# Optimization experiments

Hardware: AMD Instinct MI355X
Metric: run time of the kernel (lower is better)

The kernel has to match this reference:

```python
import jax, jax.numpy as jnp
import numpy as np

IN_C = 256
OUT_C = 256
HID = IN_C * 2
N_POINTS = 262144
N_NODES = 8192
B = 16
MAX_NODES = 512
EPS = 1e-5


def _mlp(h, w1, b1, g1, be1, w2, b2):
    # PyG MLP([C, 2C, out], norm='layer_norm'): lin -> layernorm -> relu -> (dropout, eval=identity) -> lin
    h = h @ w1 + b1
    mu = jnp.mean(h, axis=-1, keepdims=True)
    var = jnp.var(h, axis=-1, keepdims=True)
    h = (h - mu) * jax.lax.rsqrt(var + EPS) * g1 + be1
    h = jax.nn.relu(h)
    return h @ w2 + b2


def setup_inputs() -> dict:
    key = jax.random.key(0)
    ks = jax.random.split(key, 16)
    x = jax.random.normal(ks[0], (N_POINTS, IN_C), dtype=jnp.float32)
    f_point_batches = jnp.sort(jax.random.randint(ks[1], (N_POINTS,), 0, N_NODES)).astype(jnp.int32)
    # equal-sized graphs (16 graphs x 512 nodes), sorted as torch.split/pad_sequence assume
    g_node_batches = jnp.repeat(jnp.arange(B, dtype=jnp.int32), MAX_NODES)
    s = 1.0 / np.sqrt(IN_C)
    s2 = 1.0 / np.sqrt(HID)
    def lin(k, fan_in, shape, scale):
        return jax.random.uniform(k, shape, jnp.float32, -scale, scale)
    params = {}
    for i, name in enumerate(['Wq', 'Wk']):
        base = 2 + i * 6
        params[f'{name}_w1'] = lin(ks[base + 0], IN_C, (IN_C, HID), s)
        params[f'{name}_b1'] = lin(ks[base + 1], IN_C, (HID,), s)
        params[f'{name}_g1'] = jnp.ones((HID,), jnp.float32)
        params[f'{name}_be1'] = jnp.zeros((HID,), jnp.float32)
        params[f'{name}_w2'] = lin(ks[base + 2], HID, (HID, OUT_C), s2)
        params[f'{name}_b2'] = lin(ks[base + 3], HID, (OUT_C,), s2)
    return dict(x=x, f_point_batches=f_point_batches, g_node_batches=g_node_batches,
                num_graphs=B, max_nodes=MAX_NODES, **params)


def reference(x, f_point_batches, g_node_batches, num_graphs, max_nodes,
              Wq_w1, Wq_b1, Wq_g1, Wq_be1, Wq_w2, Wq_b2,
              Wk_w1, Wk_b1, Wk_g1, Wk_be1, Wk_w2, Wk_b2):
    n_nodes = g_node_batches.shape[0]
    C = x.shape[1]
    # scatter_mean over points -> per-node feature means [n_nodes, C]
    sums = jax.ops.segment_sum(x, f_point_batches, num_segments=n_nodes)
    cnt = jax.ops.segment_sum(jnp.ones((x.shape[0],), x.dtype), f_point_batches, num_segments=n_nodes)
    mean = sums / jnp.maximum(cnt, 1.0)[:, None]
    # ragged split by graph + pad_sequence -> [B, max_nodes, C]
    starts = jnp.searchsorted(g_node_batches, jnp.arange(num_graphs, dtype=g_node_batches.dtype))
    pos = jnp.arange(n_nodes) - starts[g_node_batches]
    padded = jnp.zeros((num_graphs, max_nodes, C), x.dtype).at[g_node_batches, pos].set(mean, mode='drop')
    q = _mlp(padded, Wq_w1, Wq_b1, Wq_g1, Wq_be1, Wq_w2, Wq_b2)  # [B, MAXN, out]
    k = _mlp(padded, Wk_w1, Wk_b1, Wk_g1, Wk_be1, Wk_w2, Wk_b2)
    return jnp.einsum('bnd,bmd->bnm', q, k)  # bmm(q, k^T)
```

## Files before the change

### kernel.cpp

```cpp
#include <hip/hip_runtime.h>
#include <hip/hip_bf16.h>

#define N_POINTS 262144
#define N_NODES  8192
#define IN_C     256
#define HID      512
#define OUT_C    256
#define NB       16
#define MAXN     512
#define EPSV     1e-5f
#define NPB      16

typedef __attribute__((ext_vector_type(8))) short short8;
typedef __attribute__((ext_vector_type(4))) float f32x4;
#define MFMA16(a, b, c) __builtin_amdgcn_mfma_f32_16x16x32_bf16((a), (b), (c), 0, 0, 0)


__global__ __launch_bounds__(256) void prelude_k(
    const int* __restrict__ fpb, int* __restrict__ starts,
    const float* __restrict__ W1q, const float* __restrict__ W1k,
    const float* __restrict__ W2q, const float* __restrict__ W2k,
    __hip_bfloat16* __restrict__ P1q, __hip_bfloat16* __restrict__ P1k,
    __hip_bfloat16* __restrict__ P2q, __hip_bfloat16* __restrict__ P2k)
{
  if (blockIdx.x < 1024) {
    const int i = blockIdx.x * 256 + threadIdx.x;
    const int cur = fpb[i];
    const int prev = (i == 0) ? -1 : fpb[i - 1];
    for (int n = prev + 1; n <= cur; ++n) starts[n] = i;
    if (i == N_POINTS - 1)
      for (int n = cur + 1; n <= N_NODES; ++n) starts[n] = N_POINTS;
    return;
  }
  const int bid = blockIdx.x - 1024;
  const int sel = bid >> 6;
  const float* W; __hip_bfloat16* P; int N;
  switch (sel) {
    case 0:  W = W1q; P = P1q; N = HID;   break;
    case 1:  W = W1k; P = P1k; N = HID;   break;
    case 2:  W = W2q; P = P2q; N = OUT_C; break;
    default: W = W2k; P = P2k; N = OUT_C; break;
  }
  const int idx = (bid & 63) * 256 + threadIdx.x;
  const int NF = N >> 4;
  const int lane = idx & 63;
  const int nf = (idx >> 6) % NF;
  const int ks = idx / (64 * NF);
  const int k0 = ks * 32 + (lane >> 4) * 8;
  const int n  = nf * 16 + (lane & 15);
  __hip_bfloat16 tmp[8];
  #pragma unroll
  for (int j = 0; j < 8; ++j) tmp[j] = __float2bfloat16(W[(size_t)(k0 + j) * N + n]);
  *(uint4*)(P + (size_t)idx * 8) = *(uint4*)tmp;
}

__global__ __launch_bounds__(512, 4) void fused_mlp_k(
    const float* __restrict__ x, const int* __restrict__ starts,
    const __hip_bfloat16* __restrict__ P1q, const __hip_bfloat16* __restrict__ P2q,
    const float* __restrict__ b1q, const float* __restrict__ g1q,
    const float* __restrict__ be1q, const float* __restrict__ b2q,
    const __hip_bfloat16* __restrict__ P1k, const __hip_bfloat16* __restrict__ P2k,
    const float* __restrict__ b1k, const float* __restrict__ g1k,
    const float* __restrict__ be1k, const float* __restrict__ b2k,
    __hip_bfloat16* __restrict__ qo, __hip_bfloat16* __restrict__ ko)
{
  const int n0 = blockIdx.x * NPB;
  const int t = threadIdx.x;
  const int w = t >> 6, l = t & 63, lg = l >> 4, lm = l & 15;
  const int h = w >> 2;
  const int c = w & 3;

  const __hip_bfloat16* P1 = h ? P1k : P1q;
  const __hip_bfloat16* P2 = h ? P2k : P2q;
  const float* b1  = h ? b1k  : b1q;
  const float* g1  = h ? g1k  : g1q;
  const float* be1 = h ? be1k : be1q;
  const float* b2  = h ? b2k  : b2q;
  __hip_bfloat16* out = h ? ko : qo;

  __shared__ __hip_bfloat16 As[NPB * 264];
  __shared__ __hip_bfloat16 Hs[2][NPB * 520];
  __shared__ float lnp[8][NPB][2];

  #pragma unroll
  for (int i = 0; i < 2; ++i) {
    const int nl = w * 2 + i;
    const int node = n0 + nl;
    const int s_ = starts[node], e_ = starts[node + 1];
    float4 a0 = make_float4(0.f, 0.f, 0.f, 0.f);
    float4 a1 = a0, a2 = a0, a3 = a0;
    int r = s_;
    for (; r + 4 <= e_; r += 4) {
      float4 v0 = *(const float4*)(x + (size_t)(r + 0) * IN_C + l * 4);
      float4 v1 = *(const float4*)(x + (size_t)(r + 1) * IN_C + l * 4);
      float4 v2 = *(const float4*)(x + (size_t)(r + 2) * IN_C + l * 4);
      float4 v3 = *(const float4*)(x + (size_t)(r + 3) * IN_C + l * 4);
      a0.x += v0.x; a0.y += v0.y; a0.z += v0.z; a0.w += v0.w;
      a1.x += v1.x; a1.y += v1.y; a1.z += v1.z; a1.w += v1.w;
      a2.x += v2.x; a2.y += v2.y; a2.z += v2.z; a2.w += v2.w;
      a3.x += v3.x; a3.y += v3.y; a3.z += v3.z; a3.w += v3.w;
    }
    for (; r < e_; ++r) {
      float4 v = *(const float4*)(x + (size_t)r * IN_C + l * 4);
      a0.x += v.x; a0.y += v.y; a0.z += v.z; a0.w += v.w;
    }
    a0.x += a1.x + a2.x + a3.x;
    a0.y += a1.y + a2.y + a3.y;
    a0.z += a1.z + a2.z + a3.z;
    a0.w += a1.w + a2.w + a3.w;
    const int cnt = e_ - s_;
    const float inv = cnt > 0 ? 1.0f / (float)cnt : 0.0f;
    __hip_bfloat16 o[4];
    o[0] = __float2bfloat16(a0.x * inv);
    o[1] = __float2bfloat16(a0.y * inv);
    o[2] = __float2bfloat16(a0.z * inv);
    o[3] = __float2bfloat16(a0.w * inv);
    *(uint2*)(As + nl * 264 + l * 4) = *(uint2*)o;
  }
  __syncthreads();

  f32x4 acc1[8];
  #pragma unroll
  for (int nj = 0; nj < 8; ++nj)
    #pragma unroll
    for (int r = 0; r < 4; ++r) acc1[nj][r] = 0.f;

  for (int ks = 0; ks < 8; ++ks) {
    short8 a = *(const short8*)(As + lm * 264 + ks * 32 + lg * 8);
    const __hip_bfloat16* bp = P1 + ((size_t)(ks * 32 + c * 8) * 64 + l) * 8;
    #pragma unroll
    for (int nj = 0; nj < 8; ++nj) {
      short8 b = *(const short8*)(bp + (size_t)nj * 512);
      acc1[nj] = MFMA16(a, b, acc1[nj]);
    }
  }

  float b1v[8], g1v[8], e1v[8];
  #pragma unroll
  for (int nj = 0; nj < 8; ++nj) {
    const int col = c * 128 + nj * 16 + lm;
    b1v[nj] = b1[col]; g1v[nj] = g1[col]; e1v[nj] = be1[col];
  }
  #pragma unroll
  for (int nj = 0; nj < 8; ++nj)
    #pragma unroll
    for (int r = 0; r < 4; ++r) acc1[nj][r] += b1v[nj];

  #pragma unroll
  for (int r = 0; r < 4; ++r) {
    float s = 0.f, q = 0.f;
    #pragma unroll
    for (int nj = 0; nj < 8; ++nj) {
      const float v = acc1[nj][r];
      s += v; q += v * v;
    }
    #pragma unroll
    for (int off = 1; off < 16; off <<= 1) {
      s += __shfl_xor(s, off);
      q += __shfl_xor(q, off);
    }
    if (lm == 0) {
      const int row = lg * 4 + r;
      lnp[w][row][0] = s;
      lnp[w][row][1] = q;
    }
  }
  __syncthreads();

  #pragma unroll
  for (int r = 0; r < 4; ++r) {
    const int row = lg * 4 + r;
    float S = 0.f, Q = 0.f;
    #pragma unroll
    for (int w2 = 0; w2 < 4; ++w2) {
      S += lnp[h * 4 + w2][row][0];
      Q += lnp[h * 4 + w2][row][1];
    }
    const float mu = S * (1.0f / HID);
    const float rs = rsqrtf(Q * (1.0f / HID) - mu * mu + EPSV);
    #pragma unroll
    for (int nj = 0; nj < 8; ++nj) {
      const float y = (acc1[nj][r] - mu) * rs * g1v[nj] + e1v[nj];
      Hs[h][row * 520 + c * 128 + nj * 16 + lm] = __float2bfloat16(fmaxf(y, 0.f));
    }
  }
  __syncthreads();

  f32x4 acc2[4];
  #pragma unroll
  for (int nj = 0; nj < 4; ++nj)
    #pragma unroll
    for (int r = 0; r < 4; ++r) acc2[nj][r] = 0.f;

  for (int ks = 0; ks < 16; ++ks) {
    short8 a = *(const short8*)(Hs[h] + lm * 520 + ks * 32 + lg * 8);
    const __hip_bfloat16* bp = P2 + ((size_t)(ks * 16 + c * 4) * 64 + l) * 8;
    #pragma unroll
    for (int nj = 0; nj < 4; ++nj) {
      short8 b = *(const short8*)(bp + (size_t)nj * 512);
      acc2[nj] = MFMA16(a, b, acc2[nj]);
    }
  }

  float b2v[4];
  #pragma unroll
  for (int nj = 0; nj < 4; ++nj) b2v[nj] = b2[c * 64 + nj * 16 + lm];
  #pragma unroll
  for (int nj = 0; nj < 4; ++nj)
    #pragma unroll
    for (int r = 0; r < 4; ++r) {
      const int row = n0 + lg * 4 + r;
      const int col = c * 64 + nj * 16 + lm;
      out[(size_t)row * OUT_C + col] = __float2bfloat16(acc2[nj][r] + b2v[nj]);
    }
}

__global__ __launch_bounds__(256, 4) void bmm_k(
    const __hip_bfloat16* __restrict__ q, const __hip_bfloat16* __restrict__ k,
    float* __restrict__ out)
{
  const int b  = blockIdx.z;
  const int n0 = blockIdx.x * 64;
  const int m0 = blockIdx.y * 64;
  const int t = threadIdx.x;
  const int w = t >> 6, l = t & 63, lg = l >> 4, lm = l & 15;

  const __hip_bfloat16* qb = q + ((size_t)b * MAXN + n0 + w * 16) * OUT_C;
  const __hip_bfloat16* kb = k + ((size_t)b * MAXN + m0) * OUT_C;

  f32x4 acc[4];
  #pragma unroll
  for (int nj = 0; nj < 4; ++nj)
    #pragma unroll
    for (int r = 0; r < 4; ++r) acc[nj][r] = 0.f;

  for (int ks = 0; ks < 8; ++ks) {
    short8 a = *(const short8*)(qb + (size_t)lm * OUT_C + ks * 32 + lg * 8);
    #pragma unroll
    for (int nj = 0; nj < 4; ++nj) {
      short8 bb = *(const short8*)(kb + (size_t)(nj * 16 + lm) * OUT_C + ks * 32 + lg * 8);
      acc[nj] = MFMA16(a, bb, acc[nj]);
    }
  }

  #pragma unroll
  for (int nj = 0; nj < 4; ++nj)
    #pragma unroll
    for (int r = 0; r < 4; ++r) {
      const int nrow = n0 + w * 16 + lg * 4 + r;
      const int mcol = m0 + nj * 16 + lm;
      out[((size_t)b * MAXN + nrow) * MAXN + mcol] = acc[nj][r];
    }
}

extern "C" void kernel_launch(void* const* d_in, const int* in_sizes, int n_in,
                              void* d_out, int out_size, void* d_ws, size_t ws_size,
                              hipStream_t stream)
{
  const float* x   = (const float*)d_in[0];
  const int*   fpb = (const int*)d_in[1];
  const float* Wq_w1  = (const float*)d_in[5];
  const float* Wq_b1  = (const float*)d_in[6];
  const float* Wq_g1  = (const float*)d_in[7];
  const float* Wq_be1 = (const float*)d_in[8];
  const float* Wq_w2  = (const float*)d_in[9];
  const float* Wq_b2  = (const float*)d_in[10];
  const float* Wk_w1  = (const float*)d_in[11];
  const float* Wk_b1  = (const float*)d_in[12];
  const float* Wk_g1  = (const float*)d_in[13];
  const float* Wk_be1 = (const float*)d_in[14];
  const float* Wk_w2  = (const float*)d_in[15];
  const float* Wk_b2  = (const float*)d_in[16];

  __hip_bfloat16* ws = (__hip_bfloat16*)d_ws;
  __hip_bfloat16* P1q  = ws;
  __hip_bfloat16* P1k  = P1q + 131072;
  __hip_bfloat16* P2q  = P1k + 131072;
  __hip_bfloat16* P2k  = P2q + 131072;
  __hip_bfloat16* qo   = P2k + 131072;
  __hip_bfloat16* ko   = qo + 2097152;
  int* starts = (int*)(ko + 2097152);
  float* out = (float*)d_out;

  prelude_k<<<1280, 256, 0, stream>>>(fpb, starts,
      Wq_w1, Wk_w1, Wq_w2, Wk_w2, P1q, P1k, P2q, P2k);
  fused_mlp_k<<<N_NODES / NPB, 512, 0, stream>>>(
      x, starts, P1q, P2q, Wq_b1, Wq_g1, Wq_be1, Wq_b2,
      P1k, P2k, Wk_b1, Wk_g1, Wk_be1, Wk_b2, qo, ko);
  bmm_k<<<dim3(8, 8, NB), 256, 0, stream>>>(qo, ko, out);
}
```

Before: 89.92 us.

## Warp-specialize fused MLP into producer and consumer waves with double-buffered tiles

The fused MLP kernel now runs 1024-thread blocks split into 8 producer waves that compute scatter-mean node features and 8 consumer waves that run the two MFMA GEMMs with layernorm. Each block handles two 16-node tiles, double-buffered in shared memory, so the memory-bound gather of x for the next tile overlaps with the matrix math of the previous one. The cost is halving the number of blocks, adding extra barriers per iteration, and a pipeline prologue and epilogue where half the waves sit idle. Occupancy may also drop because of the larger block and shared memory footprint.

```diff
diff --git a/kernel.cpp b/kernel.cpp
--- a/kernel.cpp
+++ b/kernel.cpp
@@ -13,6 +13,7 @@
 
 typedef __attribute__((ext_vector_type(8))) short short8;
 typedef __attribute__((ext_vector_type(4))) float f32x4;
+typedef __attribute__((ext_vector_type(4))) float f4v;
 #define MFMA16(a, b, c) __builtin_amdgcn_mfma_f32_16x16x32_bf16((a), (b), (c), 0, 0, 0)
 
 
@@ -54,7 +55,23 @@
   *(uint4*)(P + (size_t)idx * 8) = *(uint4*)tmp;
 }
 
-__global__ __launch_bounds__(512, 4) void fused_mlp_k(
+__device__ __forceinline__ void accum_rows(
+    const float* __restrict__ x, int lo, int hi, int l,
+    f4v& a0, f4v& a1, f4v& a2, f4v& a3)
+{
+  int r = lo;
+  for (; r + 4 <= hi; r += 4) {
+    f4v v0 = *(const f4v*)(x + (size_t)(r + 0) * IN_C + l * 4);
+    f4v v1 = *(const f4v*)(x + (size_t)(r + 1) * IN_C + l * 4);
+    f4v v2 = *(const f4v*)(x + (size_t)(r + 2) * IN_C + l * 4);
+    f4v v3 = *(const f4v*)(x + (size_t)(r + 3) * IN_C + l * 4);
+    a0 += v0; a1 += v1; a2 += v2; a3 += v3;
+  }
+  for (; r < hi; ++r)
+    a0 += *(const f4v*)(x + (size_t)r * IN_C + l * 4);
+}
+
+__global__ __launch_bounds__(1024) void fused_mlp_k(
     const float* __restrict__ x, const int* __restrict__ starts,
     const __hip_bfloat16* __restrict__ P1q, const __hip_bfloat16* __restrict__ P2q,
     const float* __restrict__ b1q, const float* __restrict__ g1q,
@@ -64,155 +81,169 @@
     const float* __restrict__ be1k, const float* __restrict__ b2k,
     __hip_bfloat16* __restrict__ qo, __hip_bfloat16* __restrict__ ko)
 {
-  const int n0 = blockIdx.x * NPB;
   const int t = threadIdx.x;
-  const int w = t >> 6, l = t & 63, lg = l >> 4, lm = l & 15;
-  const int h = w >> 2;
-  const int c = w & 3;
+  const int wv = t >> 6;
+  const int l = t & 63, lg = l >> 4, lm = l & 15;
+  const bool prod = wv < 8;
+  const int pw = wv & 7;
+  const int cw = wv & 7;
+  const int h = cw >> 2;
+  const int c = cw & 3;
+  const int n0b = blockIdx.x * (2 * NPB);
+
+  __shared__ __hip_bfloat16 As[2][NPB * 264];
+  __shared__ __hip_bfloat16 Hs[2][NPB * 520];
+  __shared__ float lnp[8][NPB][2];
 
   const __hip_bfloat16* P1 = h ? P1k : P1q;
   const __hip_bfloat16* P2 = h ? P2k : P2q;
-  const float* b1  = h ? b1k  : b1q;
-  const float* g1  = h ? g1k  : g1q;
-  const float* be1 = h ? be1k : be1q;
-  const float* b2  = h ? b2k  : b2q;
-  __hip_bfloat16* out = h ? ko : qo;
-
-  __shared__ __hip_bfloat16 As[NPB * 264];
-  __shared__ __hip_bfloat16 Hs[2][NPB * 520];
-  __shared__ float lnp[8][NPB][2];
-
-  #pragma unroll
-  for (int i = 0; i < 2; ++i) {
-    const int nl = w * 2 + i;
-    const int node = n0 + nl;
-    const int s_ = starts[node], e_ = starts[node + 1];
-    float4 a0 = make_float4(0.f, 0.f, 0.f, 0.f);
-    float4 a1 = a0, a2 = a0, a3 = a0;
-    int r = s_;
-    for (; r + 4 <= e_; r += 4) {
-      float4 v0 = *(const float4*)(x + (size_t)(r + 0) * IN_C + l * 4);
-      float4 v1 = *(const float4*)(x + (size_t)(r + 1) * IN_C + l * 4);
-      float4 v2 = *(const float4*)(x + (size_t)(r + 2) * IN_C + l * 4);
-      float4 v3 = *(const float4*)(x + (size_t)(r + 3) * IN_C + l * 4);
-      a0.x += v0.x; a0.y += v0.y; a0.z += v0.z; a0.w += v0.w;
-      a1.x += v1.x; a1.y += v1.y; a1.z += v1.z; a1.w += v1.w;
-      a2.x += v2.x; a2.y += v2.y; a2.z += v2.z; a2.w += v2.w;
-      a3.x += v3.x; a3.y += v3.y; a3.z += v3.z; a3.w += v3.w;
-    }
-    for (; r < e_; ++r) {
-      float4 v = *(const float4*)(x + (size_t)r * IN_C + l * 4);
-      a0.x += v.x; a0.y += v.y; a0.z += v.z; a0.w += v.w;
-    }
-    a0.x += a1.x + a2.x + a3.x;
-    a0.y += a1.y + a2.y + a3.y;
-    a0.z += a1.z + a2.z + a3.z;
-    a0.w += a1.w + a2.w + a3.w;
-    const int cnt = e_ - s_;
-    const float inv = cnt > 0 ? 1.0f / (float)cnt : 0.0f;
-    __hip_bfloat16 o[4];
-    o[0] = __float2bfloat16(a0.x * inv);
-    o[1] = __float2bfloat16(a0.y * inv);
-    o[2] = __float2bfloat16(a0.z * inv);
-    o[3] = __float2bfloat16(a0.w * inv);
-    *(uint2*)(As + nl * 264 + l * 4) = *(uint2*)o;
-  }
-  __syncthreads();
-
-  f32x4 acc1[8];
-  #pragma unroll
-  for (int nj = 0; nj < 8; ++nj)
-    #pragma unroll
-    for (int r = 0; r < 4; ++r) acc1[nj][r] = 0.f;
-
-  for (int ks = 0; ks < 8; ++ks) {
-    short8 a = *(const short8*)(As + lm * 264 + ks * 32 + lg * 8);
-    const __hip_bfloat16* bp = P1 + ((size_t)(ks * 32 + c * 8) * 64 + l) * 8;
+  __hip_bfloat16* outp = h ? ko : qo;
+
+  float b1v[8], g1v[8], e1v[8], b2v[4];
+  if (!prod) {
+    const float* b1  = h ? b1k  : b1q;
+    const float* g1  = h ? g1k  : g1q;
+    const float* be1 = h ? be1k : be1q;
+    const float* b2  = h ? b2k  : b2q;
     #pragma unroll
     for (int nj = 0; nj < 8; ++nj) {
-      short8 b = *(const short8*)(bp + (size_t)nj * 512);
-      acc1[nj] = MFMA16(a, b, acc1[nj]);
-    }
-  }
-
-  float b1v[8], g1v[8], e1v[8];
-  #pragma unroll
-  for (int nj = 0; nj < 8; ++nj) {
-    const int col = c * 128 + nj * 16 + lm;
-    b1v[nj] = b1[col]; g1v[nj] = g1[col]; e1v[nj] = be1[col];
-  }
-  #pragma unroll
-  for (int nj = 0; nj < 8; ++nj)
-    #pragma unroll
-    for (int r = 0; r < 4; ++r) acc1[nj][r] += b1v[nj];
-
-  #pragma unroll
-  for (int r = 0; r < 4; ++r) {
-    float s = 0.f, q = 0.f;
-    #pragma unroll
-    for (int nj = 0; nj < 8; ++nj) {
-      const float v = acc1[nj][r];
-      s += v; q += v * v;
-    }
-    #pragma unroll
-    for (int off = 1; off < 16; off <<= 1) {
-      s += __shfl_xor(s, off);
-      q += __shfl_xor(q, off);
-    }
-    if (lm == 0) {
-      const int row = lg * 4 + r;
-      lnp[w][row][0] = s;
-      lnp[w][row][1] = q;
-    }
-  }
-  __syncthreads();
-
-  #pragma unroll
-  for (int r = 0; r < 4; ++r) {
-    const int row = lg * 4 + r;
-    float S = 0.f, Q = 0.f;
-    #pragma unroll
-    for (int w2 = 0; w2 < 4; ++w2) {
-      S += lnp[h * 4 + w2][row][0];
-      Q += lnp[h * 4 + w2][row][1];
-    }
-    const float mu = S * (1.0f / HID);
-    const float rs = rsqrtf(Q * (1.0f / HID) - mu * mu + EPSV);
-    #pragma unroll
-    for (int nj = 0; nj < 8; ++nj) {
-      const float y = (acc1[nj][r] - mu) * rs * g1v[nj] + e1v[nj];
-      Hs[h][row * 520 + c * 128 + nj * 16 + lm] = __float2bfloat16(fmaxf(y, 0.f));
-    }
-  }
-  __syncthreads();
-
-  f32x4 acc2[4];
-  #pragma unroll
-  for (int nj = 0; nj < 4; ++nj)
-    #pragma unroll
-    for (int r = 0; r < 4; ++r) acc2[nj][r] = 0.f;
-
-  for (int ks = 0; ks < 16; ++ks) {
-    short8 a = *(const short8*)(Hs[h] + lm * 520 + ks * 32 + lg * 8);
-    const __hip_bfloat16* bp = P2 + ((size_t)(ks * 16 + c * 4) * 64 + l) * 8;
-    #pragma unroll
-    for (int nj = 0; nj < 4; ++nj) {
-      short8 b = *(const short8*)(bp + (size_t)nj * 512);
-      acc2[nj] = MFMA16(a, b, acc2[nj]);
-    }
-  }
-
-  float b2v[4];
-  #pragma unroll
-  for (int nj = 0; nj < 4; ++nj) b2v[nj] = b2[c * 64 + nj * 16 + lm];
-  #pragma unroll
-  for (int nj = 0; nj < 4; ++nj)
-    #pragma unroll
-    for (int r = 0; r < 4; ++r) {
-      const int row = n0 + lg * 4 + r;
-      const int col = c * 64 + nj * 16 + lm;
-      out[(size_t)row * OUT_C + col] = __float2bfloat16(acc2[nj][r] + b2v[nj]);
-    }
+      const int col = c * 128 + nj * 16 + lm;
+      b1v[nj] = b1[col]; g1v[nj] = g1[col]; e1v[nj] = be1[col];
+    }
+    #pragma unroll
+    for (int nj = 0; nj < 4; ++nj) b2v[nj] = b2[c * 64 + nj * 16 + lm];
+  }
+
+  for (int iter = 0; iter <= 2; ++iter) {
+    const int buf = iter & 1;
+    const int pbuf = buf ^ 1;
+
+    int sB = 0, eB = 0, mB = 0;
+    f4v pb0 = (f4v)0.f, pb1 = (f4v)0.f, pb2 = (f4v)0.f, pb3 = (f4v)0.f;
+    f32x4 acc1[8];
+
+    if (prod) {
+      if (iter < 2) {
+        const int tn0 = n0b + iter * NPB;
+        const int nodeA = tn0 + pw * 2;
+        const int sA = starts[nodeA], eA = starts[nodeA + 1];
+        f4v a0 = (f4v)0.f, a1 = (f4v)0.f, a2 = (f4v)0.f, a3 = (f4v)0.f;
+        accum_rows(x, sA, eA, l, a0, a1, a2, a3);
+        a0 += a1 + a2 + a3;
+        const int cnt = eA - sA;
+        const float inv = cnt > 0 ? 1.0f / (float)cnt : 0.0f;
+        __hip_bfloat16 o[4];
+        o[0] = __float2bfloat16(a0.x * inv);
+        o[1] = __float2bfloat16(a0.y * inv);
+        o[2] = __float2bfloat16(a0.z * inv);
+        o[3] = __float2bfloat16(a0.w * inv);
+        *(uint2*)(&As[buf][(pw * 2) * 264 + l * 4]) = *(uint2*)o;
+        const int nodeB = nodeA + 1;
+        sB = starts[nodeB]; eB = starts[nodeB + 1];
+        mB = sB + (((eB - sB) >> 1) & ~3);
+      }
+    } else if (iter > 0) {
+      #pragma unroll
+      for (int nj = 0; nj < 8; ++nj)
+        #pragma unroll
+        for (int r = 0; r < 4; ++r) acc1[nj][r] = 0.f;
+      for (int ks = 0; ks < 8; ++ks) {
+        short8 a = *(const short8*)(&As[pbuf][lm * 264 + ks * 32 + lg * 8]);
+        const __hip_bfloat16* bp = P1 + ((size_t)(ks * 32 + c * 8) * 64 + l) * 8;
+        #pragma unroll
+        for (int nj = 0; nj < 8; ++nj) {
+          short8 b = *(const short8*)(bp + (size_t)nj * 512);
+          acc1[nj] = MFMA16(a, b, acc1[nj]);
+        }
+      }
+      #pragma unroll
+      for (int nj = 0; nj < 8; ++nj)
+        #pragma unroll
+        for (int r = 0; r < 4; ++r) acc1[nj][r] += b1v[nj];
+      #pragma unroll
+      for (int r = 0; r < 4; ++r) {
+        float s = 0.f, q = 0.f;
+        #pragma unroll
+        for (int nj = 0; nj < 8; ++nj) {
+          const float v = acc1[nj][r];
+          s += v; q += v * v;
+        }
+        #pragma unroll
+        for (int off = 1; off < 16; off <<= 1) {
+          s += __shfl_xor(s, off);
+          q += __shfl_xor(q, off);
+        }
+        if (lm == 0) {
+          lnp[cw][lg * 4 + r][0] = s;
+          lnp[cw][lg * 4 + r][1] = q;
+        }
+      }
+    }
+    __syncthreads();
+
+    if (prod) {
+      if (iter < 2) accum_rows(x, sB, mB, l, pb0, pb1, pb2, pb3);
+    } else if (iter > 0) {
+      #pragma unroll
+      for (int r = 0; r < 4; ++r) {
+        const int row = lg * 4 + r;
+        float S = 0.f, Q = 0.f;
+        #pragma unroll
+        for (int w2 = 0; w2 < 4; ++w2) {
+          S += lnp[h * 4 + w2][row][0];
+          Q += lnp[h * 4 + w2][row][1];
+        }
+        const float mu = S * (1.0f / HID);
+        const float rs = rsqrtf(Q * (1.0f / HID) - mu * mu + EPSV);
+        #pragma unroll
+        for (int nj = 0; nj < 8; ++nj) {
+          const float y = (acc1[nj][r] - mu) * rs * g1v[nj] + e1v[nj];
+          Hs[h][row * 520 + c * 128 + nj * 16 + lm] = __float2bfloat16(fmaxf(y, 0.f));
+        }
+      }
+    }
+    __syncthreads();
+
+    if (prod) {
+      if (iter < 2) {
+        accum_rows(x, mB, eB, l, pb0, pb1, pb2, pb3);
+        pb0 += pb1 + pb2 + pb3;
+        const int cnt = eB - sB;
+        const float inv = cnt > 0 ? 1.0f / (float)cnt : 0.0f;
+        __hip_bfloat16 o[4];
+        o[0] = __float2bfloat16(pb0.x * inv);
+        o[1] = __float2bfloat16(pb0.y * inv);
+        o[2] = __float2bfloat16(pb0.z * inv);
+        o[3] = __float2bfloat16(pb0.w * inv);
+        *(uint2*)(&As[buf][(pw * 2 + 1) * 264 + l * 4]) = *(uint2*)o;
+      }
+    } else if (iter > 0) {
+      f32x4 acc2[4];
+      #pragma unroll
+      for (int nj = 0; nj < 4; ++nj)
+        #pragma unroll
+        for (int r = 0; r < 4; ++r) acc2[nj][r] = 0.f;
+      for (int ks = 0; ks < 16; ++ks) {
+        short8 a = *(const short8*)(&Hs[h][lm * 520 + ks * 32 + lg * 8]);
+        const __hip_bfloat16* bp = P2 + ((size_t)(ks * 16 + c * 4) * 64 + l) * 8;
+        #pragma unroll
+        for (int nj = 0; nj < 4; ++nj) {
+          short8 b = *(const short8*)(bp + (size_t)nj * 512);
+          acc2[nj] = MFMA16(a, b, acc2[nj]);
+        }
+      }
+      const int tn0p = n0b + (iter - 1) * NPB;
+      #pragma unroll
+      for (int nj = 0; nj < 4; ++nj)
+        #pragma unroll
+        for (int r = 0; r < 4; ++r) {
+          const int row = tn0p + lg * 4 + r;
+          const int col = c * 64 + nj * 16 + lm;
+          outp[(size_t)row * OUT_C + col] = __float2bfloat16(acc2[nj][r] + b2v[nj]);
+        }
+    }
+    __syncthreads();
+  }
 }
 
 __global__ __launch_bounds__(256, 4) void bmm_k(
@@ -284,7 +315,7 @@
 
   prelude_k<<<1280, 256, 0, stream>>>(fpb, starts,
       Wq_w1, Wk_w1, Wq_w2, Wk_w2, P1q, P1k, P2q, P2k);
-  fused_mlp_k<<<N_NODES / NPB, 512, 0, stream>>>(
+  fused_mlp_k<<<N_NODES / (2 * NPB), 1024, 0, stream>>>(
       x, starts, P1q, P2q, Wq_b1, Wq_g1, Wq_be1, Wq_b2,
       P1k, P2k, Wk_b1, Wk_g1, Wk_be1, Wk_b2, qo, ko);
   bmm_k<<<dim3(8, 8, NB), 256, 0, stream>>>(qo, ko, out);
```

After: 249.9 us. +178.0%, slower.
